# Kernel tuning notes

Measured on AMD Instinct MI355X. Metric: run time of the kernel, lower is better.

Reference implementation:

```python
import jax, jax.numpy as jnp
import numpy as np

N = 100000
E = 1600000
D_IN, D_HID, D_OUT = 128, 256, 128


def setup_inputs() -> dict:
    key = jax.random.key(0)
    ks = jax.random.split(key, 8)
    x = jax.random.normal(ks[0], (N, D_IN), dtype=jnp.float32)
    edge_index = jax.random.randint(ks[1], (2, E), 0, N, dtype=jnp.int64)
    # PyG SAGEConv params: lin_l (applied to aggregated neighbors, has bias),
    # lin_r (applied to root/self, no bias). Stored as [in, out] for x @ W.
    s0 = 1.0 / np.sqrt(D_IN)
    s1 = 1.0 / np.sqrt(D_HID)
    Wl0 = jax.random.uniform(ks[2], (D_IN, D_HID), jnp.float32, -s0, s0)
    bl0 = jnp.zeros((D_HID,), jnp.float32)
    Wr0 = jax.random.uniform(ks[3], (D_IN, D_HID), jnp.float32, -s0, s0)
    Wl1 = jax.random.uniform(ks[4], (D_HID, D_OUT), jnp.float32, -s1, s1)
    bl1 = jnp.zeros((D_OUT,), jnp.float32)
    Wr1 = jax.random.uniform(ks[5], (D_HID, D_OUT), jnp.float32, -s1, s1)
    return {"x": x, "edge_index": edge_index, "Wl0": Wl0, "bl0": bl0,
            "Wr0": Wr0, "Wl1": Wl1, "bl1": bl1, "Wr1": Wr1}


def _sage_conv(x, src, dst, W_l, b_l, W_r, num_nodes):
    # mean-aggregate source features at destination nodes
    msg = x[src]                                         # [E, d] gather
    agg = jax.ops.segment_sum(msg, dst, num_segments=num_nodes)  # [N, d]
    deg = jax.ops.segment_sum(jnp.ones((src.shape[0],), x.dtype), dst,
                              num_segments=num_nodes)    # [N]
    agg = agg / jnp.maximum(deg, 1.0)[:, None]
    return agg @ W_l + b_l + x @ W_r                     # [N, out]


def reference(x, edge_index, Wl0, bl0, Wr0, Wl1, bl1, Wr1):
    src, dst = edge_index[0], edge_index[1]
    n = x.shape[0]
    h = _sage_conv(x, src, dst, Wl0, bl0, Wr0, n)
    h = jax.nn.relu(h)  # dropout is identity in eval mode
    out = _sage_conv(h, src, dst, Wl1, bl1, Wr1, n)
    return out
```

## Files before the change

kernel.cpp:

```cpp
#include <hip/hip_runtime.h>

typedef short bf16x8 __attribute__((ext_vector_type(8)));
typedef float f32x4 __attribute__((ext_vector_type(4)));
typedef unsigned int uint;
typedef unsigned short ushort;
typedef ushort u16x8 __attribute__((ext_vector_type(8)));
typedef uint u32x2 __attribute__((ext_vector_type(2)));
typedef uint u32x4 __attribute__((ext_vector_type(4)));

#define NBLK 256
#define LCAP 24576

__device__ inline ushort f2bf(float f) {
    uint u = __builtin_bit_cast(uint, f);
    uint r = u + 0x7fffu + ((u >> 16) & 1u);
    return (ushort)(r >> 16);
}
__device__ inline float bf2f(uint lo16) {
    uint u = lo16 << 16;
    return __builtin_bit_cast(float, u);
}

__global__ void p1_kernel(const int* __restrict__ dst, int* __restrict__ ghist,
                          int E, int CE, int NB) {
    __shared__ int hist[512];
    int tid = threadIdx.x;
    for (int b = tid; b < NB; b += 256) hist[b] = 0;
    __syncthreads();
    int start = blockIdx.x * CE, end = min(E, start + CE);
    for (int e = start + tid; e < end; e += 256) {
        int d = dst[e];
        atomicAdd(&hist[d >> 8], 1);
    }
    __syncthreads();
    for (int b = tid; b < NB; b += 256) ghist[(size_t)b * NBLK + blockIdx.x] = hist[b];
}

__global__ void scan1_kernel(const int* __restrict__ cnt, int* __restrict__ rs,
                             int* __restrict__ bsum, int n) {
    __shared__ int tmp[256];
    int tid = threadIdx.x;
    int idx = blockIdx.x * 256 + tid;
    int v = (idx < n) ? cnt[idx] : 0;
    tmp[tid] = v;
    __syncthreads();
#pragma unroll
    for (int off = 1; off < 256; off <<= 1) {
        int t = (tid >= off) ? tmp[tid - off] : 0;
        __syncthreads();
        tmp[tid] += t;
        __syncthreads();
    }
    if (idx < n) rs[idx] = tmp[tid] - v;
    if (tid == 255) bsum[blockIdx.x] = tmp[255];
}

__global__ void scan2_kernel(int* __restrict__ bsum, int nb) {
    __shared__ int tmp[512];
    int tid = threadIdx.x;
    int v = (tid < nb) ? bsum[tid] : 0;
    tmp[tid] = v;
    __syncthreads();
#pragma unroll
    for (int off = 1; off < 512; off <<= 1) {
        int t = (tid >= off) ? tmp[tid - off] : 0;
        __syncthreads();
        tmp[tid] += t;
        __syncthreads();
    }
    if (tid < nb) bsum[tid] = tmp[tid] - v;
}

__global__ void scan3_kernel(int* __restrict__ rs, const int* __restrict__ bsum, int n, int E) {
    int idx = blockIdx.x * 256 + threadIdx.x;
    if (idx < n) rs[idx] += bsum[blockIdx.x];
    if (idx == 0) rs[n] = E;
}

__global__ void p3_kernel(const int* __restrict__ src, const int* __restrict__ dst,
                          const int* __restrict__ goff, uint* __restrict__ ebuck,
                          int E, int CE, int NB) {
    __shared__ int cur[512];
    int tid = threadIdx.x;
    for (int b = tid; b < NB; b += 256) cur[b] = goff[(size_t)b * NBLK + blockIdx.x];
    __syncthreads();
    int start = blockIdx.x * CE, end = min(E, start + CE);
    for (int e = start + tid; e < end; e += 256) {
        int d = dst[e];
        int s = src[e];
        int slot = atomicAdd(&cur[d >> 8], 1);
        ebuck[slot] = ((uint)(d & 255) << 17) | (uint)s;
    }
}

__global__ void p4_kernel(const uint* __restrict__ ebuck, const int* __restrict__ goff,
                          int* __restrict__ rs, int* __restrict__ nbr, int n, int E, int NB) {
    __shared__ uint ebuf[LCAP];
    __shared__ int cnt[256];
    __shared__ int cur[256];
    int tid = threadIdx.x;
    int b = blockIdx.x;
    int d0 = b << 8;
    int eb = goff[(size_t)b * NBLK];
    int ee = (b == NB - 1) ? E : goff[(size_t)(b + 1) * NBLK];
    cnt[tid] = 0;
    __syncthreads();
    int m = ee - eb;
    for (int i = tid; i < m; i += 256) {
        uint v = ebuck[eb + i];
        if (i < LCAP) ebuf[i] = v;
        atomicAdd(&cnt[v >> 17], 1);
    }
    __syncthreads();
    int v0 = cnt[tid];
    cur[tid] = v0;
    __syncthreads();
#pragma unroll
    for (int off = 1; off < 256; off <<= 1) {
        int t = (tid >= off) ? cur[tid - off] : 0;
        __syncthreads();
        cur[tid] += t;
        __syncthreads();
    }
    int excl = cur[tid] - v0;
    int node = d0 + tid;
    if (node < n) rs[node] = eb + excl;
    if (b == NB - 1 && tid == 0) rs[n] = E;
    __syncthreads();
    cur[tid] = eb + excl;
    __syncthreads();
    for (int i = tid; i < m; i += 256) {
        uint v = (i < LCAP) ? ebuf[i] : ebuck[eb + i];
        int p = atomicAdd(&cur[v >> 17], 1);
        nbr[p] = (int)(v & 0x1FFFFu);
    }
}


__global__ void convx_kernel(const float* __restrict__ x, ushort* __restrict__ a1, int n) {
    int i = blockIdx.x * blockDim.x + threadIdx.x;
    int total = n * 32;
    if (i >= total) return;
    int row = i >> 5, q = i & 31;
    float4 v = *(const float4*)(x + (size_t)row * 128 + q * 4);
    ushort4 o;
    o.x = f2bf(v.x); o.y = f2bf(v.y); o.z = f2bf(v.z); o.w = f2bf(v.w);
    *(ushort4*)(a1 + (size_t)row * 256 + q * 4) = o;
}

__global__ void packw_kernel(const float* __restrict__ Wa, const float* __restrict__ Wb,
                             ushort* __restrict__ out, int mode) {
    int tile = blockIdx.x;
    int l = threadIdx.x;
    int cb = tile >> 3, ks = tile & 7;
    int col = cb * 16 + (l & 15);
    int k0 = ks * 32 + ((l >> 4) * 8);
    ushort vals[8];
#pragma unroll
    for (int j = 0; j < 8; j++) {
        int k = k0 + j;
        float f;
        if (mode == 0)
            f = (k < 128) ? Wa[(size_t)k * 256 + col] : Wb[(size_t)(k - 128) * 256 + col];
        else
            f = (col < 128) ? Wa[(size_t)k * 128 + col] : Wb[(size_t)k * 128 + (col - 128)];
        vals[j] = f2bf(f);
    }
    ushort* dst = out + ((size_t)tile * 64 + l) * 8;
#pragma unroll
    for (int j = 0; j < 8; j++) dst[j] = vals[j];
}

template <int LAYER>
__launch_bounds__(256, 2)
__global__ void mfma_gemm_kernel(const ushort* __restrict__ A, const ushort* __restrict__ Wp,
                                 const float* __restrict__ bias, ushort* __restrict__ out_bf,
                                 float* __restrict__ out_f, int n) {
    __shared__ unsigned char smem[65536];
    int tid = threadIdx.x;
    int l = tid & 63, w = tid >> 6;
    int row0 = blockIdx.x * 128 + w * 32;

    bf16x8 a[2][8];
#pragma unroll
    for (int g = 0; g < 2; g++) {
        int ar = row0 + g * 16 + (l & 15);
        if (ar > n - 1) ar = n - 1;
        const ushort* ap = A + (size_t)ar * 256 + ((l >> 4) * 8);
#pragma unroll
        for (int ks = 0; ks < 8; ks++) a[g][ks] = *(const bf16x8*)(ap + ks * 32);
    }

    f32x4 acc[2][16];
#pragma unroll
    for (int g = 0; g < 2; g++)
#pragma unroll
        for (int cb = 0; cb < 16; cb++) acc[g][cb] = (f32x4){0.f, 0.f, 0.f, 0.f};

    const unsigned char* wbytes = (const unsigned char*)Wp;

#pragma unroll
    for (int half = 0; half < 2; half++) {
        {
            const unsigned char* src = wbytes + half * 65536;
#pragma unroll
            for (int i = 0; i < 16; i += 4) {
                u32x4 t0 = *(const u32x4*)(src + (size_t)(i + 0) * 4096 + tid * 16);
                u32x4 t1 = *(const u32x4*)(src + (size_t)(i + 1) * 4096 + tid * 16);
                u32x4 t2 = *(const u32x4*)(src + (size_t)(i + 2) * 4096 + tid * 16);
                u32x4 t3 = *(const u32x4*)(src + (size_t)(i + 3) * 4096 + tid * 16);
                *(u32x4*)(smem + (i + 0) * 4096 + tid * 16) = t0;
                *(u32x4*)(smem + (i + 1) * 4096 + tid * 16) = t1;
                *(u32x4*)(smem + (i + 2) * 4096 + tid * 16) = t2;
                *(u32x4*)(smem + (i + 3) * 4096 + tid * 16) = t3;
            }
        }
        __syncthreads();
#pragma unroll
        for (int cb = 0; cb < 8; cb++) {
            bf16x8 b[8];
            const unsigned char* bp = smem + ((size_t)(cb * 8) * 64 + l) * 16;
#pragma unroll
            for (int ks = 0; ks < 8; ks++) b[ks] = *(const bf16x8*)(bp + (size_t)ks * 1024);
#pragma unroll
            for (int ks = 0; ks < 8; ks++) {
                acc[0][half * 8 + cb] =
                    __builtin_amdgcn_mfma_f32_16x16x32_bf16(b[ks], a[0][ks], acc[0][half * 8 + cb], 0, 0, 0);
                acc[1][half * 8 + cb] =
                    __builtin_amdgcn_mfma_f32_16x16x32_bf16(b[ks], a[1][ks], acc[1][half * 8 + cb], 0, 0, 0);
            }
        }
        __syncthreads();
    }

    if (LAYER == 0) {
        ushort* ep = (ushort*)(void*)smem + (size_t)w * (16 * 272);
#pragma unroll
        for (int g = 0; g < 2; g++) {
            int rbase = row0 + g * 16;
#pragma unroll
            for (int cb = 0; cb < 16; cb++) {
                int colb = cb * 16 + (l >> 4) * 4;
                f32x4 bv = *(const f32x4*)(bias + colb);
                f32x4 v = acc[g][cb];
                float v0 = fmaxf(v[0] + bv[0], 0.f);
                float v1 = fmaxf(v[1] + bv[1], 0.f);
                float v2 = fmaxf(v[2] + bv[2], 0.f);
                float v3 = fmaxf(v[3] + bv[3], 0.f);
                u32x2 pk;
                pk[0] = (uint)f2bf(v0) | ((uint)f2bf(v1) << 16);
                pk[1] = (uint)f2bf(v2) | ((uint)f2bf(v3) << 16);
                *(u32x2*)&ep[(l & 15) * 272 + colb] = pk;
            }
            int rr = l >> 2, q = l & 3;
            int row = rbase + rr;
#pragma unroll
            for (int rep = 0; rep < 8; rep++) {
                u16x8 vv = *(const u16x8*)&ep[rr * 272 + q * 8 + rep * 32];
                if (row < n)
                    *(u16x8*)(out_bf + (size_t)row * 256 + q * 8 + rep * 32) = vv;
            }
        }
    } else {
        ushort* ep = (ushort*)(void*)smem + (size_t)w * (16 * 136);
#pragma unroll
        for (int g = 0; g < 2; g++) {
            int rbase = row0 + g * 16;
#pragma unroll
            for (int cb = 0; cb < 8; cb++) {
                int colb = cb * 16 + (l >> 4) * 4;
                f32x4 v = acc[g][cb];
                u32x2 pk;
                pk[0] = (uint)f2bf(v[0]) | ((uint)f2bf(v[1]) << 16);
                pk[1] = (uint)f2bf(v[2]) | ((uint)f2bf(v[3]) << 16);
                *(u32x2*)&ep[(l & 15) * 136 + colb] = pk;
            }
            {
                int rr = l >> 2, q = l & 3;
                int row = rbase + rr;
#pragma unroll
                for (int rep = 0; rep < 4; rep++) {
                    u16x8 vv = *(const u16x8*)&ep[rr * 136 + q * 8 + rep * 32];
                    if (row < n)
                        *(u16x8*)(out_bf + (size_t)row * 128 + q * 8 + rep * 32) = vv;
                }
            }
            int orow = rbase + (l & 15);
#pragma unroll
            for (int cb = 8; cb < 16; cb++) {
                int colb = (cb - 8) * 16 + (l >> 4) * 4;
                f32x4 bv = *(const f32x4*)(bias + colb);
                f32x4 v = acc[g][cb];
                v[0] += bv[0]; v[1] += bv[1]; v[2] += bv[2]; v[3] += bv[3];
                if (orow < n)
                    *(f32x4*)(out_f + (size_t)orow * 128 + colb) = v;
            }
        }
    }
}

template <int ADD>
__global__ void segmean_kernel(const uint* __restrict__ fp, int half, const int* __restrict__ rs,
                               const int* __restrict__ nbr,
                               uint* __restrict__ outb, float* __restrict__ outf, int n) {
    int w = threadIdx.x >> 6;
    int l = threadIdx.x & 63;
    int i = blockIdx.x * 4 + w;
    if (i >= n) return;
    int b = rs[i], e = rs[i + 1];
    const uint* fpl = fp + l;
    float a0 = 0.f, a1 = 0.f;
    int j = b;
    for (; j + 8 <= e; j += 8) {
        int s[8];
#pragma unroll
        for (int q = 0; q < 8; q++) s[q] = nbr[j + q];
        uint v[8];
#pragma unroll
        for (int q = 0; q < 8; q++) v[q] = fpl[(size_t)s[q] * half];
#pragma unroll
        for (int q = 0; q < 8; q++) {
            a0 += bf2f(v[q] & 0xffffu);
            a1 += bf2f(v[q] >> 16);
        }
    }
    for (; j + 2 <= e; j += 2) {
        int s0 = nbr[j], s1 = nbr[j + 1];
        uint v0 = fpl[(size_t)s0 * half];
        uint v1 = fpl[(size_t)s1 * half];
        a0 += bf2f(v0 & 0xffffu) + bf2f(v1 & 0xffffu);
        a1 += bf2f(v0 >> 16) + bf2f(v1 >> 16);
    }
    for (; j < e; j++) {
        uint v = fpl[(size_t)nbr[j] * half];
        a0 += bf2f(v & 0xffffu);
        a1 += bf2f(v >> 16);
    }
    int dg = e - b;
    float inv = 1.0f / (float)(dg > 1 ? dg : 1);
    a0 *= inv; a1 *= inv;
    if (ADD) {
        outf[(size_t)i * 2 * half + 2 * l] += a0;
        outf[(size_t)i * 2 * half + 2 * l + 1] += a1;
    } else {
        outb[(size_t)i * half + l] = ((uint)f2bf(a1) << 16) | (uint)f2bf(a0);
    }
}


extern "C" void kernel_launch(void* const* d_in, const int* in_sizes, int n_in,
                              void* d_out, int out_size, void* d_ws, size_t ws_size,
                              hipStream_t stream) {
    const float* x = (const float*)d_in[0];
    const int* ei = (const int*)d_in[1];
    const float* Wl0 = (const float*)d_in[2];
    const float* bl0 = (const float*)d_in[3];
    const float* Wr0 = (const float*)d_in[4];
    const float* Wl1 = (const float*)d_in[5];
    const float* bl1 = (const float*)d_in[6];
    const float* Wr1 = (const float*)d_in[7];
    float* outp = (float*)d_out;

    int n = in_sizes[0] / 128;
    int E = in_sizes[1] / 2;
    const int* srcv = ei;
    const int* dstv = ei + E;

    int NB = (n + 255) >> 8;
    int NG = NB * NBLK;
    int CE = (E + NBLK - 1) / NBLK;

    char* w = (char*)d_ws;
    auto align = [](size_t v) { return (v + 255) & ~(size_t)255; };
    size_t off = 0;
    int* rs    = (int*)(w + off); off = align(off + (size_t)(n + 1) * 4);
    int* bsum2 = (int*)(w + off); off = align(off + (size_t)512 * 4);
    int* ghist = (int*)(w + off); off = align(off + (size_t)(NG + 1) * 4);
    int* goff  = (int*)(w + off); off = align(off + (size_t)(NG + 1) * 4);
    uint* ebuck = (uint*)(w + off); off = align(off + (size_t)E * 4);
    int* nbr   = (int*)(w + off); off = align(off + (size_t)E * 4);
    ushort* a1  = (ushort*)(w + off); off = align(off + (size_t)n * 256 * 2);
    ushort* hb  = (ushort*)(w + off); off = align(off + (size_t)n * 256 * 2);
    ushort* zb  = (ushort*)(w + off); off = align(off + (size_t)n * 128 * 2);
    ushort* w1p = (ushort*)(w + off); off = align(off + (size_t)256 * 256 * 2);
    ushort* w2p = (ushort*)(w + off); off = align(off + (size_t)256 * 256 * 2);
    (void)ws_size; (void)n_in; (void)out_size;

    int nb2 = (NG + 255) / 256;

    p1_kernel<<<NBLK, 256, 0, stream>>>(dstv, ghist, E, CE, NB);
    scan1_kernel<<<nb2, 256, 0, stream>>>(ghist, goff, bsum2, NG);
    scan2_kernel<<<1, 512, 0, stream>>>(bsum2, nb2);
    scan3_kernel<<<nb2, 256, 0, stream>>>(goff, bsum2, NG, E);
    p3_kernel<<<NBLK, 256, 0, stream>>>(srcv, dstv, goff, ebuck, E, CE, NB);
    p4_kernel<<<NB, 256, 0, stream>>>(ebuck, goff, rs, nbr, n, E, NB);

    convx_kernel<<<(n * 32 + 255) / 256, 256, 0, stream>>>(x, a1, n);
    packw_kernel<<<128, 64, 0, stream>>>(Wr0, Wl0, w1p, 0);
    packw_kernel<<<128, 64, 0, stream>>>(Wl1, Wr1, w2p, 1);

    int segb = (n + 3) / 4;
    int mb = (n + 127) / 128;

    segmean_kernel<0><<<segb, 256, 0, stream>>>((const uint*)a1, 128, rs, nbr,
                                                (uint*)(a1 + 128), nullptr, n);
    mfma_gemm_kernel<0><<<mb, 256, 0, stream>>>(a1, w1p, bl0, hb, nullptr, n);

    mfma_gemm_kernel<1><<<mb, 256, 0, stream>>>(hb, w2p, bl1, zb, outp, n);
    segmean_kernel<1><<<segb, 256, 0, stream>>>((const uint*)zb, 64, rs, nbr,
                                                nullptr, outp, n);
}
```

Before: 273.2 us.

## Fuse prep kernels, merge scan passes, and widen segment-mean gathers

```diff
diff --git a/kernel.cpp b/kernel.cpp
--- a/kernel.cpp
+++ b/kernel.cpp
@@ -20,138 +20,13 @@
     uint u = lo16 << 16;
     return __builtin_bit_cast(float, u);
 }
-
-__global__ void p1_kernel(const int* __restrict__ dst, int* __restrict__ ghist,
-                          int E, int CE, int NB) {
-    __shared__ int hist[512];
-    int tid = threadIdx.x;
-    for (int b = tid; b < NB; b += 256) hist[b] = 0;
-    __syncthreads();
-    int start = blockIdx.x * CE, end = min(E, start + CE);
-    for (int e = start + tid; e < end; e += 256) {
-        int d = dst[e];
-        atomicAdd(&hist[d >> 8], 1);
-    }
-    __syncthreads();
-    for (int b = tid; b < NB; b += 256) ghist[(size_t)b * NBLK + blockIdx.x] = hist[b];
-}
-
-__global__ void scan1_kernel(const int* __restrict__ cnt, int* __restrict__ rs,
-                             int* __restrict__ bsum, int n) {
-    __shared__ int tmp[256];
-    int tid = threadIdx.x;
-    int idx = blockIdx.x * 256 + tid;
-    int v = (idx < n) ? cnt[idx] : 0;
-    tmp[tid] = v;
-    __syncthreads();
-#pragma unroll
-    for (int off = 1; off < 256; off <<= 1) {
-        int t = (tid >= off) ? tmp[tid - off] : 0;
-        __syncthreads();
-        tmp[tid] += t;
-        __syncthreads();
-    }
-    if (idx < n) rs[idx] = tmp[tid] - v;
-    if (tid == 255) bsum[blockIdx.x] = tmp[255];
-}
-
-__global__ void scan2_kernel(int* __restrict__ bsum, int nb) {
-    __shared__ int tmp[512];
-    int tid = threadIdx.x;
-    int v = (tid < nb) ? bsum[tid] : 0;
-    tmp[tid] = v;
-    __syncthreads();
-#pragma unroll
-    for (int off = 1; off < 512; off <<= 1) {
-        int t = (tid >= off) ? tmp[tid - off] : 0;
-        __syncthreads();
-        tmp[tid] += t;
-        __syncthreads();
-    }
-    if (tid < nb) bsum[tid] = tmp[tid] - v;
-}
-
-__global__ void scan3_kernel(int* __restrict__ rs, const int* __restrict__ bsum, int n, int E) {
-    int idx = blockIdx.x * 256 + threadIdx.x;
-    if (idx < n) rs[idx] += bsum[blockIdx.x];
-    if (idx == 0) rs[n] = E;
-}
-
-__global__ void p3_kernel(const int* __restrict__ src, const int* __restrict__ dst,
-                          const int* __restrict__ goff, uint* __restrict__ ebuck,
-                          int E, int CE, int NB) {
-    __shared__ int cur[512];
-    int tid = threadIdx.x;
-    for (int b = tid; b < NB; b += 256) cur[b] = goff[(size_t)b * NBLK + blockIdx.x];
-    __syncthreads();
-    int start = blockIdx.x * CE, end = min(E, start + CE);
-    for (int e = start + tid; e < end; e += 256) {
-        int d = dst[e];
-        int s = src[e];
-        int slot = atomicAdd(&cur[d >> 8], 1);
-        ebuck[slot] = ((uint)(d & 255) << 17) | (uint)s;
-    }
-}
-
-__global__ void p4_kernel(const uint* __restrict__ ebuck, const int* __restrict__ goff,
-                          int* __restrict__ rs, int* __restrict__ nbr, int n, int E, int NB) {
-    __shared__ uint ebuf[LCAP];
-    __shared__ int cnt[256];
-    __shared__ int cur[256];
-    int tid = threadIdx.x;
-    int b = blockIdx.x;
-    int d0 = b << 8;
-    int eb = goff[(size_t)b * NBLK];
-    int ee = (b == NB - 1) ? E : goff[(size_t)(b + 1) * NBLK];
-    cnt[tid] = 0;
-    __syncthreads();
-    int m = ee - eb;
-    for (int i = tid; i < m; i += 256) {
-        uint v = ebuck[eb + i];
-        if (i < LCAP) ebuf[i] = v;
-        atomicAdd(&cnt[v >> 17], 1);
-    }
-    __syncthreads();
-    int v0 = cnt[tid];
-    cur[tid] = v0;
-    __syncthreads();
-#pragma unroll
-    for (int off = 1; off < 256; off <<= 1) {
-        int t = (tid >= off) ? cur[tid - off] : 0;
-        __syncthreads();
-        cur[tid] += t;
-        __syncthreads();
-    }
-    int excl = cur[tid] - v0;
-    int node = d0 + tid;
-    if (node < n) rs[node] = eb + excl;
-    if (b == NB - 1 && tid == 0) rs[n] = E;
-    __syncthreads();
-    cur[tid] = eb + excl;
-    __syncthreads();
-    for (int i = tid; i < m; i += 256) {
-        uint v = (i < LCAP) ? ebuf[i] : ebuck[eb + i];
-        int p = atomicAdd(&cur[v >> 17], 1);
-        nbr[p] = (int)(v & 0x1FFFFu);
-    }
-}
-
-
-__global__ void convx_kernel(const float* __restrict__ x, ushort* __restrict__ a1, int n) {
-    int i = blockIdx.x * blockDim.x + threadIdx.x;
-    int total = n * 32;
-    if (i >= total) return;
-    int row = i >> 5, q = i & 31;
-    float4 v = *(const float4*)(x + (size_t)row * 128 + q * 4);
-    ushort4 o;
-    o.x = f2bf(v.x); o.y = f2bf(v.y); o.z = f2bf(v.z); o.w = f2bf(v.w);
-    *(ushort4*)(a1 + (size_t)row * 256 + q * 4) = o;
-}
-
-__global__ void packw_kernel(const float* __restrict__ Wa, const float* __restrict__ Wb,
-                             ushort* __restrict__ out, int mode) {
-    int tile = blockIdx.x;
-    int l = threadIdx.x;
+__device__ inline float bf2f_hi(uint v) {
+    uint u = v & 0xffff0000u;
+    return __builtin_bit_cast(float, u);
+}
+
+__device__ inline void packw_body(const float* __restrict__ Wa, const float* __restrict__ Wb,
+                                  ushort* __restrict__ out, int mode, int tile, int l) {
     int cb = tile >> 3, ks = tile & 7;
     int col = cb * 16 + (l & 15);
     int k0 = ks * 32 + ((l >> 4) * 8);
@@ -169,6 +44,143 @@
     ushort* dst = out + ((size_t)tile * 64 + l) * 8;
 #pragma unroll
     for (int j = 0; j < 8; j++) dst[j] = vals[j];
+}
+
+__global__ void prep_kernel(const float* __restrict__ x, ushort* __restrict__ a1,
+                            const float* __restrict__ Wr0, const float* __restrict__ Wl0,
+                            ushort* __restrict__ w1p,
+                            const float* __restrict__ Wl1, const float* __restrict__ Wr1,
+                            ushort* __restrict__ w2p,
+                            const int* __restrict__ dst, int* __restrict__ ghist,
+                            int E, int CE, int NB, int n) {
+    __shared__ int hist[512];
+    int bb = blockIdx.x;
+    int tid = threadIdx.x;
+    if (bb < NBLK) {
+        for (int b = tid; b < NB; b += 256) hist[b] = 0;
+        __syncthreads();
+        int start = bb * CE, end = min(E, start + CE);
+        for (int e = start + tid; e < end; e += 256) {
+            int d = dst[e];
+            atomicAdd(&hist[d >> 8], 1);
+        }
+        __syncthreads();
+        for (int b = tid; b < NB; b += 256) ghist[(size_t)b * NBLK + bb] = hist[b];
+    } else if (bb < NBLK + 64) {
+        int r = bb - NBLK;
+        int tile = (r & 31) * 4 + (tid >> 6);
+        int l = tid & 63;
+        if (r < 32) packw_body(Wr0, Wl0, w1p, 0, tile, l);
+        else        packw_body(Wl1, Wr1, w2p, 1, tile, l);
+    } else {
+        int i = (bb - NBLK - 64) * 256 + tid;
+        int total = n * 32;
+        if (i < total) {
+            int row = i >> 5, q = i & 31;
+            float4 v = *(const float4*)(x + (size_t)row * 128 + q * 4);
+            ushort4 o;
+            o.x = f2bf(v.x); o.y = f2bf(v.y); o.z = f2bf(v.z); o.w = f2bf(v.w);
+            *(ushort4*)(a1 + (size_t)row * 256 + q * 4) = o;
+        }
+    }
+}
+
+__global__ void scan1_kernel(const int* __restrict__ cnt, int* __restrict__ rs,
+                             int* __restrict__ bsum, int n) {
+    __shared__ int tmp[256];
+    int tid = threadIdx.x;
+    int idx = blockIdx.x * 256 + tid;
+    int v = (idx < n) ? cnt[idx] : 0;
+    tmp[tid] = v;
+    __syncthreads();
+#pragma unroll
+    for (int off = 1; off < 256; off <<= 1) {
+        int t = (tid >= off) ? tmp[tid - off] : 0;
+        __syncthreads();
+        tmp[tid] += t;
+        __syncthreads();
+    }
+    if (idx < n) rs[idx] = tmp[tid] - v;
+    if (tid == 255) bsum[blockIdx.x] = tmp[255];
+}
+
+__global__ void scan23_kernel(int* __restrict__ rs, const int* __restrict__ bsum,
+                              int n, int E) {
+    __shared__ int red[256];
+    int tid = threadIdx.x;
+    int b = blockIdx.x;
+    int s = 0;
+    for (int t = tid; t < b; t += 256) s += bsum[t];
+    red[tid] = s;
+    __syncthreads();
+#pragma unroll
+    for (int off = 128; off > 0; off >>= 1) {
+        if (tid < off) red[tid] += red[tid + off];
+        __syncthreads();
+    }
+    int offv = red[0];
+    int idx = b * 256 + tid;
+    if (idx < n) rs[idx] += offv;
+    if (b == 0 && tid == 0) rs[n] = E;
+}
+
+__global__ void p3_kernel(const int* __restrict__ src, const int* __restrict__ dst,
+                          const int* __restrict__ goff, uint* __restrict__ ebuck,
+                          int E, int CE, int NB) {
+    __shared__ int cur[512];
+    int tid = threadIdx.x;
+    for (int b = tid; b < NB; b += 256) cur[b] = goff[(size_t)b * NBLK + blockIdx.x];
+    __syncthreads();
+    int start = blockIdx.x * CE, end = min(E, start + CE);
+    for (int e = start + tid; e < end; e += 256) {
+        int d = dst[e];
+        int s = src[e];
+        int slot = atomicAdd(&cur[d >> 8], 1);
+        ebuck[slot] = ((uint)(d & 255) << 17) | (uint)s;
+    }
+}
+
+__global__ void p4_kernel(const uint* __restrict__ ebuck, const int* __restrict__ goff,
+                          int* __restrict__ rs, int* __restrict__ nbr, int n, int E, int NB) {
+    __shared__ uint ebuf[LCAP];
+    __shared__ int cnt[256];
+    __shared__ int cur[256];
+    int tid = threadIdx.x;
+    int b = blockIdx.x;
+    int d0 = b << 8;
+    int eb = goff[(size_t)b * NBLK];
+    int ee = (b == NB - 1) ? E : goff[(size_t)(b + 1) * NBLK];
+    cnt[tid] = 0;
+    __syncthreads();
+    int m = ee - eb;
+    for (int i = tid; i < m; i += 256) {
+        uint v = ebuck[eb + i];
+        if (i < LCAP) ebuf[i] = v;
+        atomicAdd(&cnt[v >> 17], 1);
+    }
+    __syncthreads();
+    int v0 = cnt[tid];
+    cur[tid] = v0;
+    __syncthreads();
+#pragma unroll
+    for (int off = 1; off < 256; off <<= 1) {
+        int t = (tid >= off) ? cur[tid - off] : 0;
+        __syncthreads();
+        cur[tid] += t;
+        __syncthreads();
+    }
+    int excl = cur[tid] - v0;
+    int node = d0 + tid;
+    if (node < n) rs[node] = eb + excl;
+    if (b == NB - 1 && tid == 0) rs[n] = E;
+    __syncthreads();
+    cur[tid] = eb + excl;
+    __syncthreads();
+    for (int i = tid; i < m; i += 256) {
+        uint v = (i < LCAP) ? ebuf[i] : ebuck[eb + i];
+        int p = atomicAdd(&cur[v >> 17], 1);
+        nbr[p] = (int)(v & 0x1FFFFu);
+    }
 }
 
 template <int LAYER>
@@ -300,50 +312,64 @@
 }
 
 template <int ADD>
-__global__ void segmean_kernel(const uint* __restrict__ fp, int half, const int* __restrict__ rs,
-                               const int* __restrict__ nbr,
+__global__ void segmean_kernel(const uint* __restrict__ fp, int half ,
+                               const int* __restrict__ rs, const int* __restrict__ nbr,
                                uint* __restrict__ outb, float* __restrict__ outf, int n) {
     int w = threadIdx.x >> 6;
     int l = threadIdx.x & 63;
     int i = blockIdx.x * 4 + w;
     if (i >= n) return;
     int b = rs[i], e = rs[i + 1];
-    const uint* fpl = fp + l;
-    float a0 = 0.f, a1 = 0.f;
+    int q = l & 31;
+    int hsel = l >> 5;
+    int stride2 = half >> 1;
+    const uint2* fpq = (const uint2*)fp + q;
+    float a0 = 0.f, a1 = 0.f, a2 = 0.f, a3 = 0.f;
     int j = b;
     for (; j + 8 <= e; j += 8) {
-        int s[8];
-#pragma unroll
-        for (int q = 0; q < 8; q++) s[q] = nbr[j + q];
-        uint v[8];
-#pragma unroll
-        for (int q = 0; q < 8; q++) v[q] = fpl[(size_t)s[q] * half];
-#pragma unroll
-        for (int q = 0; q < 8; q++) {
-            a0 += bf2f(v[q] & 0xffffu);
-            a1 += bf2f(v[q] >> 16);
+        int s[4];
+#pragma unroll
+        for (int p = 0; p < 4; p++) s[p] = nbr[j + 2 * p + hsel];
+        uint2 v[4];
+#pragma unroll
+        for (int p = 0; p < 4; p++) v[p] = fpq[(size_t)s[p] * stride2];
+#pragma unroll
+        for (int p = 0; p < 4; p++) {
+            a0 += bf2f(v[p].x & 0xffffu); a1 += bf2f_hi(v[p].x);
+            a2 += bf2f(v[p].y & 0xffffu); a3 += bf2f_hi(v[p].y);
         }
     }
     for (; j + 2 <= e; j += 2) {
-        int s0 = nbr[j], s1 = nbr[j + 1];
-        uint v0 = fpl[(size_t)s0 * half];
-        uint v1 = fpl[(size_t)s1 * half];
-        a0 += bf2f(v0 & 0xffffu) + bf2f(v1 & 0xffffu);
-        a1 += bf2f(v0 >> 16) + bf2f(v1 >> 16);
-    }
-    for (; j < e; j++) {
-        uint v = fpl[(size_t)nbr[j] * half];
-        a0 += bf2f(v & 0xffffu);
-        a1 += bf2f(v >> 16);
-    }
-    int dg = e - b;
-    float inv = 1.0f / (float)(dg > 1 ? dg : 1);
-    a0 *= inv; a1 *= inv;
-    if (ADD) {
-        outf[(size_t)i * 2 * half + 2 * l] += a0;
-        outf[(size_t)i * 2 * half + 2 * l + 1] += a1;
-    } else {
-        outb[(size_t)i * half + l] = ((uint)f2bf(a1) << 16) | (uint)f2bf(a0);
+        int s = nbr[j + hsel];
+        uint2 v = fpq[(size_t)s * stride2];
+        a0 += bf2f(v.x & 0xffffu); a1 += bf2f_hi(v.x);
+        a2 += bf2f(v.y & 0xffffu); a3 += bf2f_hi(v.y);
+    }
+    if (j < e && hsel == 0) {
+        int s = nbr[j];
+        uint2 v = fpq[(size_t)s * stride2];
+        a0 += bf2f(v.x & 0xffffu); a1 += bf2f_hi(v.x);
+        a2 += bf2f(v.y & 0xffffu); a3 += bf2f_hi(v.y);
+    }
+    a0 += __shfl_xor(a0, 32);
+    a1 += __shfl_xor(a1, 32);
+    a2 += __shfl_xor(a2, 32);
+    a3 += __shfl_xor(a3, 32);
+    if (hsel == 0) {
+        int dg = e - b;
+        float inv = 1.0f / (float)(dg > 1 ? dg : 1);
+        a0 *= inv; a1 *= inv; a2 *= inv; a3 *= inv;
+        if (ADD) {
+            float* op = outf + (size_t)i * (2 * half) + q * 4;
+            f32x4 o = *(const f32x4*)op;
+            o[0] += a0; o[1] += a1; o[2] += a2; o[3] += a3;
+            *(f32x4*)op = o;
+        } else {
+            u32x2 pk;
+            pk[0] = (uint)f2bf(a0) | ((uint)f2bf(a1) << 16);
+            pk[1] = (uint)f2bf(a2) | ((uint)f2bf(a3) << 16);
+            *(u32x2*)(outb + (size_t)i * half + q * 2) = pk;
+        }
     }
 }
 
@@ -387,17 +413,14 @@
     (void)ws_size; (void)n_in; (void)out_size;
 
     int nb2 = (NG + 255) / 256;
-
-    p1_kernel<<<NBLK, 256, 0, stream>>>(dstv, ghist, E, CE, NB);
+    int ncx = (n * 32 + 255) / 256;
+
+    prep_kernel<<<NBLK + 64 + ncx, 256, 0, stream>>>(x, a1, Wr0, Wl0, w1p, Wl1, Wr1, w2p,
+                                                     dstv, ghist, E, CE, NB, n);
     scan1_kernel<<<nb2, 256, 0, stream>>>(ghist, goff, bsum2, NG);
-    scan2_kernel<<<1, 512, 0, stream>>>(bsum2, nb2);
-    scan3_kernel<<<nb2, 256, 0, stream>>>(goff, bsum2, NG, E);
+    scan23_kernel<<<nb2, 256, 0, stream>>>(goff, bsum2, NG, E);
     p3_kernel<<<NBLK, 256, 0, stream>>>(srcv, dstv, goff, ebuck, E, CE, NB);
     p4_kernel<<<NB, 256, 0, stream>>>(ebuck, goff, rs, nbr, n, E, NB);
-
-    convx_kernel<<<(n * 32 + 255) / 256, 256, 0, stream>>>(x, a1, n);
-    packw_kernel<<<128, 64, 0, stream>>>(Wr0, Wl0, w1p, 0);
-    packw_kernel<<<128, 64, 0, stream>>>(Wl1, Wr1, w2p, 1);
 
     int segb = (n + 3) / 4;
     int mb = (n + 127) / 128;
```

After: 266.6 us. -2.4%, faster.
